# Kernel optimization log

Measured on AMD Instinct MI355X. Metric: run time of the kernel, lower is better.

Reference implementation:

```python
import jax, jax.numpy as jnp
import numpy as np

K = 20
NEG_SLOPE = 0.2
BN_EPS = 1e-5


def knn_idx(x, k):
    # x: (B, C, N) -> neighbor indices (B, N, k) by largest negative sq-distance
    xt = jnp.swapaxes(x, 1, 2)                      # (B, N, C)
    inner = 2.0 * jnp.einsum('bic,bjc->bij', xt, xt)
    sq = jnp.sum(xt * xt, axis=-1)                  # (B, N)
    dist = inner - sq[:, :, None] - sq[:, None, :]  # -||xi-xj||^2
    _, idx = jax.lax.top_k(dist, k)
    return idx


def edge_feature(x, src, idx):
    # x: (B, C, N) centers; src: (B, C, M) gather source; idx: (B, N, k)
    xt = jnp.swapaxes(x, 1, 2)                      # (B, N, C)
    st = jnp.swapaxes(src, 1, 2)                    # (B, M, C)
    b = jnp.arange(xt.shape[0])[:, None, None]
    neigh = st[b, idx]                              # (B, N, k, C)
    center = xt[:, :, None, :]                      # (B, N, 1, C)
    feat = jnp.concatenate(
        [neigh - center, jnp.broadcast_to(center, neigh.shape)], axis=-1)
    return jnp.transpose(feat, (0, 3, 1, 2))        # (B, 2C, N, k)


def conv_bn_lrelu(x, w, gamma, beta):
    # 1x1 conv (no bias) + training-mode BatchNorm2d + LeakyReLU(0.2)
    y = jnp.einsum('oc,bcnk->bonk', w, x)
    mean = jnp.mean(y, axis=(0, 2, 3), keepdims=True)
    var = jnp.var(y, axis=(0, 2, 3), keepdims=True)
    y = (y - mean) * jax.lax.rsqrt(var + BN_EPS)
    y = y * gamma[None, :, None, None] + beta[None, :, None, None]
    return jnp.where(y >= 0, y, NEG_SLOPE * y)


def knn_ia_idx(x, y, k):
    # cosine-similarity KNN from x (B,Cx,N) into y (B,Cy,M), normalize over channels
    xn = x / jnp.maximum(jnp.linalg.norm(x, axis=1, keepdims=True), 1e-12)
    yn = y / jnp.maximum(jnp.linalg.norm(y, axis=1, keepdims=True), 1e-12)
    simi = jnp.einsum('bci,bcj->bij', xn, yn)       # (B, N, M)
    _, idx = jax.lax.top_k(simi, k)
    return idx


def setup_inputs() -> dict:
    key = jax.random.key(0)
    ks = jax.random.split(key, 8)
    B, N, M, EMB = 8, 1024, 1024, 512
    x = jax.random.normal(ks[0], (B, 3, N), dtype=jnp.float32)
    y = jax.random.normal(ks[1], (B, 128, M), dtype=jnp.float32)
    def w(k_, o, c):
        return jax.random.normal(k_, (o, c), dtype=jnp.float32) * (1.0 / np.sqrt(c))
    inp = {
        'x': x, 'y': y,
        'w1': w(ks[2], 64, 6),
        'w2': w(ks[3], 64, 128),
        'w3': w(ks[4], 128, 128),
        'w4': w(ks[5], 256, 256),
        'w5': w(ks[6], EMB, 512),
        'g1': jnp.ones(64), 'b1': jnp.zeros(64),
        'g2': jnp.ones(64), 'b2': jnp.zeros(64),
        'g3': jnp.ones(128), 'b3': jnp.zeros(128),
        'g4': jnp.ones(256), 'b4': jnp.zeros(256),
        'g5': jnp.ones(EMB), 'b5': jnp.zeros(EMB),
    }
    return inp


def reference(x, y, w1, w2, w3, w4, w5, g1, b1, g2, b2, g3, b3, g4, b4, g5, b5):
    # block 1
    h = conv_bn_lrelu(edge_feature(x, x, knn_idx(x, K)), w1, g1, b1)
    x1 = jnp.max(h, axis=-1)                        # (B, 64, N)
    # block 2
    h = conv_bn_lrelu(edge_feature(x1, x1, knn_idx(x1, K)), w2, g2, b2)
    x2 = jnp.max(h, axis=-1)                        # (B, 64, N)
    # block 3
    h = conv_bn_lrelu(edge_feature(x2, x2, knn_idx(x2, K)), w3, g3, b3)
    x3 = jnp.max(h, axis=-1)                        # (B, 128, N)
    # block 4: cross-attention KNN into y (cosine similarity)
    h = conv_bn_lrelu(edge_feature(x3, y, knn_ia_idx(x3, y, K)), w4, g4, b4)
    x4 = jnp.max(h, axis=-1)                        # (B, 256, N)
    # final 1x1 conv + BN + LeakyReLU on concatenated features (512 ch)
    cat = jnp.concatenate([x1, x2, x3, x4], axis=1)  # (B, 512, N)
    out = conv_bn_lrelu(cat[..., None], w5, g5, b5)[..., 0]
    return out                                       # (B, n_emb_dims, N)
```

## Files before the change

### kernel.cpp

```cpp
#include <hip/hip_runtime.h>
#include <hip/hip_bf16.h>

#define KNN 20
#define NEG_SLOPE 0.2f

constexpr int BB = 8;
constexpr int NN = 1024;
constexpr int MM = 1024;

typedef short bf16x8 __attribute__((ext_vector_type(8)));
typedef float f32x4 __attribute__((ext_vector_type(4)));
typedef double f64x4 __attribute__((ext_vector_type(4)));
typedef unsigned long long u64;

__device__ __forceinline__ u64 pack_key64(double d, int j) {
  u64 u = (u64)__double_as_longlong(d);
  u = (u & 0x8000000000000000ULL) ? ~u : (u | 0x8000000000000000ULL);
  return (u & ~(u64)1023) | (u64)(1023 - j);
}

__device__ __forceinline__ void topk20_u64(u64 (&s)[16], int lane, int* op) {
#pragma unroll
  for (int p = 1; p < 16; p <<= 1) {
#pragma unroll
    for (int k = p; k >= 1; k >>= 1) {
#pragma unroll
      for (int j = k % p; j + k < 16; j += 2 * k) {
#pragma unroll
        for (int i = 0; i < k; ++i) {
          int a = j + i, b = j + i + k;
          if (b < 16 && (a / (2 * p)) == (b / (2 * p))) {
            u64 hi = s[a] > s[b] ? s[a] : s[b];
            u64 lo = s[a] > s[b] ? s[b] : s[a];
            s[a] = hi;
            s[b] = lo;
          }
        }
      }
    }
  }
#pragma unroll
  for (int r = 0; r < KNN; ++r) {
    u64 win = s[0];
#pragma unroll
    for (int off = 32; off > 0; off >>= 1) {
      u64 o = __shfl_xor(win, off, 64);
      win = o > win ? o : win;
    }
    if (lane == 0) op[r] = 1023 - (int)(win & (u64)1023);
    if (s[0] == win) {
#pragma unroll
      for (int i = 0; i < 15; ++i) s[i] = s[i + 1];
      s[15] = 0ULL;
    }
  }
}

__global__ void k_probe_mfma(int* __restrict__ rowt, int* __restrict__ colt,
                             int* __restrict__ flag) {
  __shared__ int cnt[256];
  __shared__ int oksh;
  int tid = threadIdx.x;
  if (tid == 0) oksh = 1;
  for (int e = tid; e < 256; e += 64) cnt[e] = 0;
  __syncthreads();
  int lane = tid & 63;
  f64x4 z = {0.0, 0.0, 0.0, 0.0};
  double ai = (double)(lane & 15);
  double p3 = 1.0, p5 = 1.0;
  int kq = lane >> 4;
  for (int t = 0; t < kq; ++t) { p3 *= 3.0; p5 *= 5.0; }
  f64x4 d1 = __builtin_amdgcn_mfma_f64_16x16x4f64(ai, 1.0, z, 0, 0, 0);
  f64x4 d2 = __builtin_amdgcn_mfma_f64_16x16x4f64(1.0, ai, z, 0, 0, 0);
  f64x4 d3 = __builtin_amdgcn_mfma_f64_16x16x4f64(p3, p5, z, 0, 0, 0);
  bool ok = true;
  int ri[4], ci[4];
#pragma unroll
  for (int r = 0; r < 4; ++r) {
    double va = d1[r], vb = d2[r], vp = d3[r];
    int i = (int)(va * 0.25);
    int j = (int)(vb * 0.25);
    bool e_ok = (i >= 0) && (i < 16) && (j >= 0) && (j < 16) &&
                (va == 4.0 * (double)i) && (vb == 4.0 * (double)j) && (vp == 3616.0);
    if (e_ok) {
      atomicAdd(&cnt[i * 16 + j], 1);
    } else {
      ok = false;
      i = 0;
      j = 0;
    }
    ri[r] = i;
    ci[r] = j;
  }
  if (!ok) atomicExch(&oksh, 0);
  __syncthreads();
  bool bij = true;
  for (int e = tid; e < 256; e += 64)
    if (cnt[e] != 1) bij = false;
  if (!bij) atomicExch(&oksh, 0);
  __syncthreads();
#pragma unroll
  for (int r = 0; r < 4; ++r) {
    rowt[lane * 4 + r] = ri[r];
    colt[lane * 4 + r] = ci[r];
  }
  if (tid == 0) *flag = oksh;
}

__global__ __launch_bounds__(256) void k_transpose_d(
    const float* __restrict__ in, double* __restrict__ out, int C, int Np) {
  int total = BB * C * Np;
  for (int t = blockIdx.x * 256 + threadIdx.x; t < total; t += gridDim.x * 256) {
    int c = t % C;
    int n = (t / C) % Np;
    int b = t / (C * Np);
    out[t] = (double)in[((size_t)b * C + c) * Np + n];
  }
}

__global__ __launch_bounds__(256) void k_cvt_bf16(
    const float* __restrict__ in, __hip_bfloat16* __restrict__ out, int n) {
  int i = blockIdx.x * 256 + threadIdx.x;
  if (i < n) out[i] = __float2bfloat16(in[i]);
}

template <int RECIP>
__global__ __launch_bounds__(256) void k_rowsq(
    const double* __restrict__ A, int ld, int C, double* __restrict__ sq) {
  int p = blockIdx.x * 256 + threadIdx.x;
  if (p >= BB * NN) return;
  const double* row = A + (size_t)p * ld;
  double s = 0.0;
  for (int c = 0; c < C; ++c) { double v = row[c]; s += v * v; }
  if (RECIP) {
    sq[p] = 1.0 / fmax(sqrt(s), 1e-12);
  } else {
    sq[p] = s;
  }
}

__global__ __launch_bounds__(256) void k_knn3(
    const double* __restrict__ xs3, const double* __restrict__ sq, int* __restrict__ idx) {
  __shared__ double P[NN * 3];
  int b = blockIdx.x;
  const double* Xb = xs3 + (size_t)b * NN * 3;
  int tid = threadIdx.x;
  for (int t = tid; t < NN * 3; t += 256) P[t] = Xb[t];
  __syncthreads();
  int wave = tid >> 6, lane = tid & 63;
  int i = blockIdx.y * 4 + wave;
  double xi = P[i * 3], yi = P[i * 3 + 1], zi = P[i * 3 + 2];
  double sqi = sq[b * NN + i];
  u64 s[16];
#pragma unroll
  for (int m = 0; m < 16; ++m) {
    int j = m * 64 + lane;
    double d = fma(xi, P[j * 3], 0.0);
    d = fma(yi, P[j * 3 + 1], d);
    d = fma(zi, P[j * 3 + 2], d);
    s[m] = pack_key64(2.0 * d - sqi - sq[b * NN + j], j);
  }
  int* op = idx + ((size_t)b * NN + i) * KNN;
  topk20_u64(s, lane, op);
}

template <int MODE>
__global__ __launch_bounds__(64, 2) void k_gram_u(
    const double* __restrict__ A, int lda, const double* __restrict__ Bm, int ldb,
    const double* __restrict__ sqA, const double* __restrict__ sqB,
    u64* __restrict__ kk, int C, int b0, const int* __restrict__ rowt,
    const int* __restrict__ colt, const int* __restrict__ flag) {
  __shared__ double As[2][8][69];
  __shared__ double Bs[2][8][69];
  int bg = b0 + blockIdx.x;
  int bl = blockIdx.x;
  int j0 = blockIdx.y * 64;
  int i0 = blockIdx.z * 64;
  const double* Ab = A + (size_t)bg * NN * lda;
  const double* Bb = Bm + (size_t)bg * MM * ldb;
  int lane = threadIdx.x;
  if (*flag) {
    int lm = lane & 15, lq = lane >> 4;
    int k8 = lane & 7, r8 = lane >> 3;
    const double* pa = Ab + (size_t)(i0 + r8) * lda + k8;
    const double* pb = Bb + (size_t)(j0 + r8) * ldb + k8;
    f64x4 acc[4][4] = {};
    double ra[8], rb[8];
#pragma unroll
    for (int r = 0; r < 8; ++r) {
      ra[r] = pa[(size_t)(8 * r) * lda];
      rb[r] = pb[(size_t)(8 * r) * ldb];
    }
#pragma unroll
    for (int r = 0; r < 8; ++r) {
      As[0][k8][r8 + 8 * r] = ra[r];
      Bs[0][k8][r8 + 8 * r] = rb[r];
    }
    int nblk = C >> 3;
    for (int cb = 0; cb < nblk; ++cb) {
      int buf = cb & 1;
      bool pf = (cb + 1 < nblk);
      if (pf) {
        int c0 = (cb + 1) << 3;
#pragma unroll
        for (int r = 0; r < 8; ++r) {
          ra[r] = pa[(size_t)(8 * r) * lda + c0];
          rb[r] = pb[(size_t)(8 * r) * ldb + c0];
        }
      }
#pragma unroll
      for (int kc = 0; kc < 2; ++kc) {
        double a_[4], b_[4];
#pragma unroll
        for (int s = 0; s < 4; ++s) {
          a_[s] = As[buf][kc * 4 + lq][s * 16 + lm];
          b_[s] = Bs[buf][kc * 4 + lq][s * 16 + lm];
        }
#pragma unroll
        for (int si = 0; si < 4; ++si)
#pragma unroll
          for (int sj = 0; sj < 4; ++sj)
            acc[si][sj] = __builtin_amdgcn_mfma_f64_16x16x4f64(a_[si], b_[sj],
                                                               acc[si][sj], 0, 0, 0);
      }
      if (pf) {
        int nb = buf ^ 1;
#pragma unroll
        for (int r = 0; r < 8; ++r) {
          As[nb][k8][r8 + 8 * r] = ra[r];
          Bs[nb][k8][r8 + 8 * r] = rb[r];
        }
      }
    }
    int rta[4], cta[4];
#pragma unroll
    for (int r = 0; r < 4; ++r) {
      rta[r] = rowt[lane * 4 + r];
      cta[r] = colt[lane * 4 + r];
    }
#pragma unroll
    for (int si = 0; si < 4; ++si) {
#pragma unroll
      for (int sj = 0; sj < 4; ++sj) {
#pragma unroll
        for (int r = 0; r < 4; ++r) {
          int i = i0 + si * 16 + rta[r];
          int j = j0 + sj * 16 + cta[r];
          double v = acc[si][sj][r];
          if (MODE == 1)
            v = 2.0 * v - sqA[(size_t)bg * NN + i] - sqB[(size_t)bg * MM + j];
          if (MODE == 2) v = v * sqA[(size_t)bg * NN + i] * sqB[(size_t)bg * MM + j];
          kk[((size_t)bl * NN + i) * MM + j] = pack_key64(v, j);
        }
      }
    }
  } else {
    int lr = lane >> 3, lc = lane & 7;
    double acc2[8][8] = {};
    for (int c0 = 0; c0 < C; c0 += 8) {
      if (c0) __syncthreads();
      for (int r = 0; r < 8; ++r) {
        int li = lane + r * 64;
        int row = li >> 3, k = li & 7;
        As[0][k][row] = Ab[(size_t)(i0 + row) * lda + c0 + k];
        Bs[0][k][row] = Bb[(size_t)(j0 + row) * ldb + c0 + k];
      }
      __syncthreads();
#pragma unroll
      for (int k = 0; k < 8; ++k) {
        double a_[8], b_[8];
#pragma unroll
        for (int t = 0; t < 8; ++t) {
          a_[t] = As[0][k][lr * 8 + t];
          b_[t] = Bs[0][k][lc * 8 + t];
        }
#pragma unroll
        for (int ii = 0; ii < 8; ++ii)
#pragma unroll
          for (int jj = 0; jj < 8; ++jj)
            acc2[ii][jj] = fma(a_[ii], b_[jj], acc2[ii][jj]);
      }
    }
    for (int ii = 0; ii < 8; ++ii) {
      int i = i0 + lr * 8 + ii;
      double qa = sqA[(size_t)bg * NN + i];
      for (int jj = 0; jj < 8; ++jj) {
        int j = j0 + lc * 8 + jj;
        double v = acc2[ii][jj];
        if (MODE == 1) v = 2.0 * v - qa - sqB[(size_t)bg * MM + j];
        if (MODE == 2) v = v * qa * sqB[(size_t)bg * MM + j];
        kk[((size_t)bl * NN + i) * MM + j] = pack_key64(v, j);
      }
    }
  }
}

__global__ __launch_bounds__(64, 2) void k_gram_sym(
    const double* __restrict__ A, int lda, const double* __restrict__ sqA,
    u64* __restrict__ kk, int C, int b0, const int* __restrict__ rowt,
    const int* __restrict__ colt, const int* __restrict__ flag) {
  __shared__ double As[2][8][69];
  __shared__ double Bs[2][8][69];
  int bg = b0 + blockIdx.x;
  int bl = blockIdx.x;
  int p = blockIdx.y;
  int r = (int)((sqrtf(8.f * p + 1.f) - 1.f) * 0.5f);
  while ((r + 1) * (r + 2) / 2 <= p) ++r;
  while (r * (r + 1) / 2 > p) --r;
  int cc = p - r * (r + 1) / 2;
  int i0 = r * 64, j0 = cc * 64;
  const double* Ab = A + (size_t)bg * NN * lda;
  int lane = threadIdx.x;
  if (*flag) {
    int lm = lane & 15, lq = lane >> 4;
    int k8 = lane & 7, r8 = lane >> 3;
    const double* pa = Ab + (size_t)(i0 + r8) * lda + k8;
    const double* pb = Ab + (size_t)(j0 + r8) * lda + k8;
    f64x4 acc[4][4] = {};
    double ra[8], rb[8];
#pragma unroll
    for (int r_ = 0; r_ < 8; ++r_) {
      ra[r_] = pa[(size_t)(8 * r_) * lda];
      rb[r_] = pb[(size_t)(8 * r_) * lda];
    }
#pragma unroll
    for (int r_ = 0; r_ < 8; ++r_) {
      As[0][k8][r8 + 8 * r_] = ra[r_];
      Bs[0][k8][r8 + 8 * r_] = rb[r_];
    }
    int nblk = C >> 3;
    for (int cb = 0; cb < nblk; ++cb) {
      int buf = cb & 1;
      bool pf = (cb + 1 < nblk);
      if (pf) {
        int c0 = (cb + 1) << 3;
#pragma unroll
        for (int r_ = 0; r_ < 8; ++r_) {
          ra[r_] = pa[(size_t)(8 * r_) * lda + c0];
          rb[r_] = pb[(size_t)(8 * r_) * lda + c0];
        }
      }
#pragma unroll
      for (int kc = 0; kc < 2; ++kc) {
        double a_[4], b_[4];
#pragma unroll
        for (int s = 0; s < 4; ++s) {
          a_[s] = As[buf][kc * 4 + lq][s * 16 + lm];
          b_[s] = Bs[buf][kc * 4 + lq][s * 16 + lm];
        }
#pragma unroll
        for (int si = 0; si < 4; ++si)
#pragma unroll
          for (int sj = 0; sj < 4; ++sj)
            acc[si][sj] = __builtin_amdgcn_mfma_f64_16x16x4f64(a_[si], b_[sj],
                                                               acc[si][sj], 0, 0, 0);
      }
      if (pf) {
        int nb = buf ^ 1;
#pragma unroll
        for (int r_ = 0; r_ < 8; ++r_) {
          As[nb][k8][r8 + 8 * r_] = ra[r_];
          Bs[nb][k8][r8 + 8 * r_] = rb[r_];
        }
      }
    }
    int rta[4], cta[4];
#pragma unroll
    for (int r_ = 0; r_ < 4; ++r_) {
      rta[r_] = rowt[lane * 4 + r_];
      cta[r_] = colt[lane * 4 + r_];
    }
    bool mir = (i0 != j0);
#pragma unroll
    for (int si = 0; si < 4; ++si) {
#pragma unroll
      for (int sj = 0; sj < 4; ++sj) {
#pragma unroll
        for (int r_ = 0; r_ < 4; ++r_) {
          int i = i0 + si * 16 + rta[r_];
          int j = j0 + sj * 16 + cta[r_];
          double v = 2.0 * acc[si][sj][r_] - sqA[(size_t)bg * NN + i] -
                     sqA[(size_t)bg * NN + j];
          kk[((size_t)bl * NN + i) * MM + j] = pack_key64(v, j);
          if (mir) kk[((size_t)bl * NN + j) * MM + i] = pack_key64(v, i);
        }
      }
    }
  } else {
    int lr = lane >> 3, lc = lane & 7;
    double acc2[8][8] = {};
    for (int c0 = 0; c0 < C; c0 += 8) {
      if (c0) __syncthreads();
      for (int r_ = 0; r_ < 8; ++r_) {
        int li = lane + r_ * 64;
        int row = li >> 3, k = li & 7;
        As[0][k][row] = Ab[(size_t)(i0 + row) * lda + c0 + k];
        Bs[0][k][row] = Ab[(size_t)(j0 + row) * lda + c0 + k];
      }
      __syncthreads();
#pragma unroll
      for (int k = 0; k < 8; ++k) {
        double a_[8], b_[8];
#pragma unroll
        for (int t = 0; t < 8; ++t) {
          a_[t] = As[0][k][lr * 8 + t];
          b_[t] = Bs[0][k][lc * 8 + t];
        }
#pragma unroll
        for (int ii = 0; ii < 8; ++ii)
#pragma unroll
          for (int jj = 0; jj < 8; ++jj)
            acc2[ii][jj] = fma(a_[ii], b_[jj], acc2[ii][jj]);
      }
    }
    bool mir = (i0 != j0);
    for (int ii = 0; ii < 8; ++ii) {
      int i = i0 + lr * 8 + ii;
      double qa = sqA[(size_t)bg * NN + i];
      for (int jj = 0; jj < 8; ++jj) {
        int j = j0 + lc * 8 + jj;
        double v = 2.0 * acc2[ii][jj] - qa - sqA[(size_t)bg * NN + j];
        kk[((size_t)bl * NN + i) * MM + j] = pack_key64(v, j);
        if (mir) kk[((size_t)bl * NN + j) * MM + i] = pack_key64(v, i);
      }
    }
  }
}

__global__ __launch_bounds__(256) void k_topk(const u64* __restrict__ kk,
                                              int* __restrict__ idx, int b0) {
  int wave = threadIdx.x >> 6;
  int lane = threadIdx.x & 63;
  int bl = blockIdx.x;
  int row = blockIdx.y * 4 + wave;
  const u64* rp = kk + ((size_t)bl * NN + row) * MM;
  u64 s[16];
#pragma unroll
  for (int m = 0; m < 16; ++m) s[m] = rp[m * 64 + lane];
  int* op = idx + ((size_t)(b0 + bl) * NN + row) * KNN;
  topk20_u64(s, lane, op);
}

__global__ __launch_bounds__(256) void k_featmm2(
    const double* __restrict__ src0, int ld0, int Np0,
    const double* __restrict__ src1, int ld1,
    const float* __restrict__ w, int CW,
    double* __restrict__ out0, double* __restrict__ out1, int C, int O,
    const int* __restrict__ rowt, const int* __restrict__ colt,
    const int* __restrict__ flag) {
  __shared__ double As[16][68];
  __shared__ double Ws[16][68];
  int nbo = O >> 6;
  int b = blockIdx.x;
  int mode = blockIdx.y >= nbo;
  int o0 = (blockIdx.y - (mode ? nbo : 0)) * 64;
  int j0 = blockIdx.z * 64;
  const double* src = mode ? src1 : src0;
  int lds_ = mode ? ld1 : ld0;
  int Np = mode ? NN : Np0;
  double* out = mode ? out1 : out0;
  int tid = threadIdx.x;
  const double* Sb = src + (size_t)b * Np * lds_;
  if (*flag) {
    int lane = tid & 63, wv = tid >> 6;
    int lm = lane & 15, lq = lane >> 4;
    f64x4 acc[4] = {};
    for (int c0 = 0; c0 < C; c0 += 16) {
      if (c0) __syncthreads();
      for (int r = 0; r < 4; ++r) {
        int li = tid + r * 256;
        int row = li >> 4, k = li & 15;
        int c = c0 + k;
        As[k][row] = (c < C) ? Sb[(size_t)(j0 + row) * lds_ + c] : 0.0;
        double wvv = 0.0;
        if (c < C) {
          const float* wr = w + (size_t)(o0 + row) * CW;
          wvv = (mode == 0) ? (double)wr[c] : ((double)wr[C + c] - (double)wr[c]);
        }
        Ws[k][row] = wvv;
      }
      __syncthreads();
#pragma unroll
      for (int kc = 0; kc < 4; ++kc) {
        double a = As[kc * 4 + lq][wv * 16 + lm];
#pragma unroll
        for (int t = 0; t < 4; ++t) {
          double bb = Ws[kc * 4 + lq][t * 16 + lm];
          acc[t] = __builtin_amdgcn_mfma_f64_16x16x4f64(a, bb, acc[t], 0, 0, 0);
        }
      }
    }
    int rta[4], cta[4];
#pragma unroll
    for (int r = 0; r < 4; ++r) {
      rta[r] = rowt[lane * 4 + r];
      cta[r] = colt[lane * 4 + r];
    }
#pragma unroll
    for (int t = 0; t < 4; ++t) {
#pragma unroll
      for (int r = 0; r < 4; ++r) {
        int j = j0 + wv * 16 + rta[r];
        int o = o0 + t * 16 + cta[r];
        out[((size_t)b * Np + j) * O + o] = acc[t][r];
      }
    }
  } else {
    int tx = tid & 15, ty = tid >> 4;
    double acc[4][4] = {};
    for (int c0 = 0; c0 < C; c0 += 16) {
      if (c0) __syncthreads();
      for (int r = 0; r < 4; ++r) {
        int li = tid + r * 256;
        int row = li >> 4, k = li & 15;
        int c = c0 + k;
        As[k][row] = (c < C) ? Sb[(size_t)(j0 + row) * lds_ + c] : 0.0;
        double wvv = 0.0;
        if (c < C) {
          const float* wr = w + (size_t)(o0 + row) * CW;
          wvv = (mode == 0) ? (double)wr[c] : ((double)wr[C + c] - (double)wr[c]);
        }
        Ws[k][row] = wvv;
      }
      __syncthreads();
#pragma unroll
      for (int k = 0; k < 16; ++k) {
        double a_[4], b_[4];
#pragma unroll
        for (int ii = 0; ii < 4; ++ii) a_[ii] = As[k][ty * 4 + ii];
#pragma unroll
        for (int jj = 0; jj < 4; ++jj) b_[jj] = Ws[k][tx * 4 + jj];
#pragma unroll
        for (int ii = 0; ii < 4; ++ii)
#pragma unroll
          for (int jj = 0; jj < 4; ++jj)
            acc[ii][jj] = fma(a_[ii], b_[jj], acc[ii][jj]);
      }
    }
    for (int ii = 0; ii < 4; ++ii) {
      int j = j0 + ty * 4 + ii;
      double* op = &out[((size_t)b * Np + j) * O + o0 + tx * 4];
      double2 v0, v1;
      v0.x = acc[ii][0];
      v0.y = acc[ii][1];
      v1.x = acc[ii][2];
      v1.y = acc[ii][3];
      *(double2*)op = v0;
      *(double2*)(op + 2) = v1;
    }
  }
}

__global__ __launch_bounds__(64, 2) void k_gemm5_mfma(
    const __hip_bfloat16* __restrict__ cath, const __hip_bfloat16* __restrict__ w5h,
    float* __restrict__ out) {
  int b = blockIdx.x;
  int j0 = blockIdx.y * 64;
  int o0 = blockIdx.z * 64;
  int lane = threadIdx.x;
  int m = lane & 15;
  int quad = lane >> 4;
  const __hip_bfloat16* arow = cath + ((size_t)(b * NN + j0 + m)) * 512 + quad * 8;
  const __hip_bfloat16* brow = w5h + ((size_t)(o0 + m)) * 512 + quad * 8;
  f32x4 acc[4][4] = {};
#pragma unroll
  for (int c0 = 0; c0 < 512; c0 += 32) {
    bf16x8 a[4], bb[4];
#pragma unroll
    for (int s = 0; s < 4; ++s) {
      a[s] = *(const bf16x8*)(arow + (size_t)s * 16 * 512 + c0);
      bb[s] = *(const bf16x8*)(brow + (size_t)s * 16 * 512 + c0);
    }
#pragma unroll
    for (int si = 0; si < 4; ++si)
#pragma unroll
      for (int sj = 0; sj < 4; ++sj)
        acc[si][sj] =
            __builtin_amdgcn_mfma_f32_16x16x32_bf16(a[si], bb[sj], acc[si][sj], 0, 0, 0);
  }
#pragma unroll
  for (int si = 0; si < 4; ++si) {
    float* ob = &out[((size_t)(b * NN + j0 + si * 16 + quad * 4)) * 512 + o0 + m];
#pragma unroll
    for (int sj = 0; sj < 4; ++sj)
#pragma unroll
      for (int r = 0; r < 4; ++r)
        ob[(size_t)r * 512 + sj * 16] = acc[si][sj][r];
  }
}

__global__ __launch_bounds__(256) void k_gather(
    const double* __restrict__ u, const double* __restrict__ t, const int* __restrict__ idx,
    double* __restrict__ stats, double* __restrict__ mx, int O, int srcNp) {
  __shared__ int lidx[16 * KNN];
  __shared__ double rs[256];
  __shared__ double rq[256];
  int b = blockIdx.x;
  int n0 = blockIdx.y * 16;
  int o0 = blockIdx.z * 64;
  int tid = threadIdx.x;
  int lane = tid & 63, nsl = tid >> 6;
  for (int w = tid; w < 16 * KNN; w += 256)
    lidx[w] = idx[((size_t)b * NN + n0) * KNN + w];
  __syncthreads();
  int oo = o0 + lane;
  double s1 = 0.0, s2 = 0.0;
  for (int ns = nsl; ns < 16; ns += 4) {
    size_t row = (size_t)b * NN + n0 + ns;
    double tv = t[row * O + oo];
    double mxv = -INFINITY;
    double a1 = 0.0, a2 = 0.0;
#pragma unroll
    for (int k = 0; k < KNN; ++k) {
      int j = lidx[ns * KNN + k];
      double yv = u[((size_t)b * srcNp + j) * O + oo] + tv;
      mxv = fmax(mxv, yv);
      a1 += yv;
      a2 = fma(yv, yv, a2);
    }
    mx[row * O + oo] = mxv;
    s1 += a1;
    s2 += a2;
  }
  rs[tid] = s1;
  rq[tid] = s2;
  __syncthreads();
  if (tid < 64) {
    s1 = rs[tid] + rs[tid + 64] + rs[tid + 128] + rs[tid + 192];
    s2 = rq[tid] + rq[tid + 64] + rq[tid + 128] + rq[tid + 192];
    atomicAdd(&stats[o0 + tid], s1);
    atomicAdd(&stats[O + o0 + tid], s2);
  }
}

__global__ __launch_bounds__(256) void k_bnapply(
    const double* __restrict__ mx, const double* __restrict__ u, const double* __restrict__ t,
    const int* __restrict__ idx, const double* __restrict__ stats,
    const float* __restrict__ gamma, const float* __restrict__ beta, double cnt,
    double* __restrict__ catd, __hip_bfloat16* __restrict__ cath, int coff, int O,
    int srcNp) {
  __shared__ double scs[256];
  __shared__ double scc[256];
  int tid = threadIdx.x;
  if (tid < O) {
    double mean = stats[tid] / cnt;
    double var = stats[O + tid] / cnt - mean * mean;
    if (var < 0.0) var = 0.0;
    double rstd = 1.0 / sqrt(var + 1e-5);
    double s = (double)gamma[tid] * rstd;
    scs[tid] = s;
    scc[tid] = (double)beta[tid] - mean * s;
  }
  __syncthreads();
  int i = blockIdx.x * 256 + tid;
  int total = BB * NN * O;
  if (i >= total) return;
  int oo = i % O;
  int n = (i / O) % NN;
  int b = i / (O * NN);
  double s = scs[oo], c = scc[oo];
  double v;
  if (s >= 0.0) {
    v = mx[i];
  } else {
    double tv = t[i];
    double mn = INFINITY;
    for (int k = 0; k < KNN; ++k) {
      int j = idx[((size_t)b * NN + n) * KNN + k];
      mn = fmin(mn, u[((size_t)b * srcNp + j) * O + oo] + tv);
    }
    v = mn;
  }
  double a = s * v + c;
  a = (a >= 0.0) ? a : 0.2 * a;
  size_t ci = ((size_t)b * NN + n) * 512 + coff + oo;
  cath[ci] = __float2bfloat16((float)a);
  if (coff < 256) catd[((size_t)b * NN + n) * 256 + coff + oo] = a;
}

__global__ __launch_bounds__(256) void k_stats512(
    const float* __restrict__ y5, double* __restrict__ stats) {
  int b = blockIdx.y;
  int n0 = blockIdx.x * 32;
  int tid = threadIdx.x;
  for (int part = 0; part < 2; ++part) {
    int oo = tid + part * 256;
    float a1 = 0.f, a2 = 0.f;
    for (int ns = 0; ns < 32; ++ns) {
      float v = y5[((size_t)b * NN + n0 + ns) * 512 + oo];
      a1 += v;
      a2 = fmaf(v, v, a2);
    }
    atomicAdd(&stats[oo], (double)a1);
    atomicAdd(&stats[512 + oo], (double)a2);
  }
}

__global__ __launch_bounds__(256) void k_final5b(
    const float* __restrict__ y5, const double* __restrict__ stats,
    const float* __restrict__ g5, const float* __restrict__ b5,
    float* __restrict__ out) {
  __shared__ float tile[64][65];
  __shared__ double scs[64];
  __shared__ double scc[64];
  int b = blockIdx.z;
  int n0 = blockIdx.x * 64;
  int o0 = blockIdx.y * 64;
  int tid = threadIdx.x;
  if (tid < 64) {
    int o = o0 + tid;
    double cnt = (double)(BB * NN);
    double mean = stats[o] / cnt;
    double var = stats[512 + o] / cnt - mean * mean;
    if (var < 0.0) var = 0.0;
    double rstd = 1.0 / sqrt(var + 1e-5);
    double s = (double)g5[o] * rstd;
    scs[tid] = s;
    scc[tid] = (double)b5[o] - mean * s;
  }
  __syncthreads();
  for (int r = 0; r < 16; ++r) {
    int li = tid + r * 256;
    int nl = li >> 6, ol = li & 63;
    float v = y5[((size_t)b * NN + n0 + nl) * 512 + o0 + ol];
    float a = (float)(scs[ol] * (double)v + scc[ol]);
    a = (a >= 0.f) ? a : NEG_SLOPE * a;
    tile[nl][ol] = a;
  }
  __syncthreads();
  for (int r = 0; r < 16; ++r) {
    int li = tid + r * 256;
    int ol = li >> 6, nl = li & 63;
    out[((size_t)b * 512 + o0 + ol) * NN + n0 + nl] = tile[nl][ol];
  }
}

extern "C" void kernel_launch(void* const* d_in, const int* in_sizes, int n_in,
                              void* d_out, int out_size, void* d_ws, size_t ws_size,
                              hipStream_t stream) {
  const float* x = (const float*)d_in[0];
  const float* y = (const float*)d_in[1];
  const float* w1 = (const float*)d_in[2];
  const float* w2 = (const float*)d_in[3];
  const float* w3 = (const float*)d_in[4];
  const float* w4 = (const float*)d_in[5];
  const float* w5 = (const float*)d_in[6];
  const float* g1 = (const float*)d_in[7];
  const float* b1 = (const float*)d_in[8];
  const float* g2 = (const float*)d_in[9];
  const float* b2 = (const float*)d_in[10];
  const float* g3 = (const float*)d_in[11];
  const float* b3 = (const float*)d_in[12];
  const float* g4 = (const float*)d_in[13];
  const float* b4 = (const float*)d_in[14];
  const float* g5 = (const float*)d_in[15];
  const float* b5 = (const float*)d_in[16];

  char* base = (char*)d_ws;
  size_t off = 0;
  auto alloc = [&](size_t bytes) -> char* {
    char* p = base + off;
    off += (bytes + 255) & ~(size_t)255;
    return p;
  };
  double* stAll = (double*)alloc(5 * 1024 * 8);
  double* sq = (double*)alloc((size_t)BB * NN * 8);
  double* rnx = (double*)alloc((size_t)BB * NN * 8);
  double* rny = (double*)alloc((size_t)BB * MM * 8);
  int* idxb = (int*)alloc((size_t)BB * NN * KNN * 4);
  int* rowt = (int*)alloc(256 * 4);
  int* colt = (int*)alloc(256 * 4);
  int* pflag = (int*)alloc(256);
  double* xs3d = (double*)alloc((size_t)BB * NN * 3 * 8);
  double* ysd = (double*)alloc((size_t)BB * MM * 128 * 8);
  double* catd = (double*)alloc((size_t)BB * NN * 256 * 8);
  __hip_bfloat16* cath = (__hip_bfloat16*)alloc((size_t)BB * NN * 512 * 2);
  __hip_bfloat16* w5h = (__hip_bfloat16*)alloc((size_t)512 * 512 * 2);
  double* uu = (double*)alloc((size_t)BB * MM * 256 * 8);
  double* tt = (double*)alloc((size_t)BB * NN * 256 * 8);
  size_t kkBatchBytes = (size_t)NN * MM * 8;
  size_t avail = (ws_size > off) ? (ws_size - off) : 0;
  int CB = (int)(avail / kkBatchBytes);
  if (CB < 1) CB = 1;
  if (CB > BB) CB = BB;
  u64* KK = (u64*)alloc((size_t)CB * kkBatchBytes);
  float* y5 = (float*)uu;
  double* mx = (double*)d_out;
  float* outp = (float*)d_out;

  const double cntE = (double)BB * NN * KNN;

  auto knn = [&](const double* A, int lda, const double* Bm, int ldb,
                 const double* sa, const double* sb, int C, int sym) {
    for (int b0 = 0; b0 < BB; b0 += CB) {
      int cb = (BB - b0 < CB) ? (BB - b0) : CB;
      if (sym) {
        k_gram_sym<<<dim3(cb, 136), 64, 0, stream>>>(A, lda, sa, KK, C, b0, rowt, colt,
                                                     pflag);
      } else {
        dim3 g(cb, MM / 64, NN / 64);
        k_gram_u<2><<<g, 64, 0, stream>>>(A, lda, Bm, ldb, sa, sb, KK, C, b0, rowt,
                                          colt, pflag);
      }
      k_topk<<<dim3(cb, 256), 256, 0, stream>>>(KK, idxb, b0);
    }
  };

  auto edge_layer = [&](const double* ctr, int ldc, const double* src, int ldsrc,
                        int srcNp, const float* w, int CW, const float* g,
                        const float* bb, int C, int O, int coff, double* st) {
    k_featmm2<<<dim3(8, 2 * (O / 64), 16), 256, 0, stream>>>(
        src, ldsrc, srcNp, ctr, ldc, w, CW, uu, tt, C, O, rowt, colt, pflag);
    k_gather<<<dim3(BB, NN / 16, O / 64), 256, 0, stream>>>(uu, tt, idxb, st, mx, O,
                                                            srcNp);
    k_bnapply<<<(BB * NN * O + 255) / 256, 256, 0, stream>>>(
        mx, uu, tt, idxb, st, g, bb, cntE, catd, cath, coff, O, srcNp);
  };

  hipMemsetAsync(stAll, 0, 5 * 1024 * 8, stream);
  k_probe_mfma<<<1, 64, 0, stream>>>(rowt, colt, pflag);
  k_transpose_d<<<96, 256, 0, stream>>>(x, xs3d, 3, NN);
  k_transpose_d<<<2048, 256, 0, stream>>>(y, ysd, 128, MM);
  k_cvt_bf16<<<1024, 256, 0, stream>>>(w5, w5h, 512 * 512);

  k_rowsq<0><<<32, 256, 0, stream>>>(xs3d, 3, 3, sq);
  k_knn3<<<dim3(BB, 256), 256, 0, stream>>>(xs3d, sq, idxb);
  edge_layer(xs3d, 3, xs3d, 3, NN, w1, 6, g1, b1, 3, 64, 0, stAll);

  k_rowsq<0><<<32, 256, 0, stream>>>(catd, 256, 64, sq);
  knn(catd, 256, catd, 256, sq, sq, 64, 1);
  edge_layer(catd, 256, catd, 256, NN, w2, 128, g2, b2, 64, 64, 64, stAll + 1024);

  k_rowsq<0><<<32, 256, 0, stream>>>(catd + 64, 256, 64, sq);
  knn(catd + 64, 256, catd + 64, 256, sq, sq, 64, 1);
  edge_layer(catd + 64, 256, catd + 64, 256, NN, w3, 128, g3, b3, 64, 128, 128,
             stAll + 2048);

  k_rowsq<1><<<32, 256, 0, stream>>>(catd + 128, 256, 128, rnx);
  k_rowsq<1><<<32, 256, 0, stream>>>(ysd, 128, 128, rny);
  knn(catd + 128, 256, ysd, 128, rnx, rny, 128, 0);
  edge_layer(catd + 128, 256, ysd, 128, MM, w4, 256, g4, b4, 128, 256, 256,
             stAll + 3072);

  double* st5 = stAll + 4096;
  k_gemm5_mfma<<<dim3(8, 16, 8), 64, 0, stream>>>(cath, w5h, y5);
  k_stats512<<<dim3(32, 8), 256, 0, stream>>>(y5, st5);
  k_final5b<<<dim3(16, 8, 8), 256, 0, stream>>>(y5, st5, g5, b5, outp);
}
```

Before: 645.2 us.

## Rewrite edge feature GEMM as single-wave 64x64 MFMA tile with register-prefetched double buffering

Changes the per-edge-layer fp64 GEMM from a 256-thread block, where each wave computed a 16x64 strip, to a single 64-lane wave that computes the whole 64x64 tile with a 4x4 grid of f64 MFMAs. It uses an 8-deep K step with double-buffered LDS, prefetching the next slab into registers while the current one is consumed. This removes block-level barriers and raises operand reuse per LDS read. The grid is reordered so the output-channel index varies fastest, for both this kernel and the gather kernel, to improve locality. The cost is heavy register use and fewer waves per block, which may reduce latency hiding.

```diff
diff --git a/kernel.cpp b/kernel.cpp
--- a/kernel.cpp
+++ b/kernel.cpp
@@ -441,112 +441,142 @@
   topk20_u64(s, lane, op);
 }
 
-__global__ __launch_bounds__(256) void k_featmm2(
+__global__ __launch_bounds__(64, 2) void k_featmm_u(
     const double* __restrict__ src0, int ld0, int Np0,
     const double* __restrict__ src1, int ld1,
     const float* __restrict__ w, int CW,
     double* __restrict__ out0, double* __restrict__ out1, int C, int O,
     const int* __restrict__ rowt, const int* __restrict__ colt,
     const int* __restrict__ flag) {
-  __shared__ double As[16][68];
-  __shared__ double Ws[16][68];
+  __shared__ double As[2][8][69];
+  __shared__ double Ws[2][8][69];
   int nbo = O >> 6;
-  int b = blockIdx.x;
-  int mode = blockIdx.y >= nbo;
-  int o0 = (blockIdx.y - (mode ? nbo : 0)) * 64;
-  int j0 = blockIdx.z * 64;
+  int mode = blockIdx.x >= nbo;
+  int o0 = (blockIdx.x - (mode ? nbo : 0)) * 64;
+  int j0 = blockIdx.y * 64;
+  int b = blockIdx.z;
   const double* src = mode ? src1 : src0;
   int lds_ = mode ? ld1 : ld0;
   int Np = mode ? NN : Np0;
   double* out = mode ? out1 : out0;
-  int tid = threadIdx.x;
   const double* Sb = src + (size_t)b * Np * lds_;
+  int lane = threadIdx.x;
   if (*flag) {
-    int lane = tid & 63, wv = tid >> 6;
     int lm = lane & 15, lq = lane >> 4;
-    f64x4 acc[4] = {};
-    for (int c0 = 0; c0 < C; c0 += 16) {
+    int k8 = lane & 7, r8 = lane >> 3;
+    const double* pa = Sb + (size_t)(j0 + r8) * lds_ + k8;
+    const float* pw = w + (size_t)(o0 + r8) * CW;
+    f64x4 acc[4][4] = {};
+    double ra[8], rb[8];
+    auto wval = [&](int radd, int c) -> double {
+      const float* wr = pw + (size_t)radd * CW;
+      return (mode == 0) ? (double)wr[c] : ((double)wr[C + c] - (double)wr[c]);
+    };
+#pragma unroll
+    for (int r = 0; r < 8; ++r) {
+      bool in = (k8 < C);
+      ra[r] = in ? pa[(size_t)(8 * r) * lds_] : 0.0;
+      rb[r] = in ? wval(8 * r, k8) : 0.0;
+    }
+#pragma unroll
+    for (int r = 0; r < 8; ++r) {
+      As[0][k8][r8 + 8 * r] = ra[r];
+      Ws[0][k8][r8 + 8 * r] = rb[r];
+    }
+    int nblk = (C + 7) >> 3;
+    for (int cb = 0; cb < nblk; ++cb) {
+      int buf = cb & 1;
+      bool pf = (cb + 1 < nblk);
+      if (pf) {
+        int c0 = (cb + 1) << 3;
+        bool in = (c0 + k8 < C);
+#pragma unroll
+        for (int r = 0; r < 8; ++r) {
+          ra[r] = in ? pa[(size_t)(8 * r) * lds_ + c0] : 0.0;
+          rb[r] = in ? wval(8 * r, c0 + k8) : 0.0;
+        }
+      }
+#pragma unroll
+      for (int kc = 0; kc < 2; ++kc) {
+        double a_[4], b_[4];
+#pragma unroll
+        for (int s = 0; s < 4; ++s) {
+          a_[s] = As[buf][kc * 4 + lq][s * 16 + lm];
+          b_[s] = Ws[buf][kc * 4 + lq][s * 16 + lm];
+        }
+#pragma unroll
+        for (int si = 0; si < 4; ++si)
+#pragma unroll
+          for (int sj = 0; sj < 4; ++sj)
+            acc[si][sj] = __builtin_amdgcn_mfma_f64_16x16x4f64(a_[si], b_[sj],
+                                                               acc[si][sj], 0, 0, 0);
+      }
+      if (pf) {
+        int nb = buf ^ 1;
+#pragma unroll
+        for (int r = 0; r < 8; ++r) {
+          As[nb][k8][r8 + 8 * r] = ra[r];
+          Ws[nb][k8][r8 + 8 * r] = rb[r];
+        }
+      }
+    }
+    int rta[4], cta[4];
+#pragma unroll
+    for (int r = 0; r < 4; ++r) {
+      rta[r] = rowt[lane * 4 + r];
+      cta[r] = colt[lane * 4 + r];
+    }
+#pragma unroll
+    for (int si = 0; si < 4; ++si) {
+#pragma unroll
+      for (int sj = 0; sj < 4; ++sj) {
+#pragma unroll
+        for (int r = 0; r < 4; ++r) {
+          int j = j0 + si * 16 + rta[r];
+          int o = o0 + sj * 16 + cta[r];
+          out[((size_t)b * Np + j) * O + o] = acc[si][sj][r];
+        }
+      }
+    }
+  } else {
+    int lr = lane >> 3, lc = lane & 7;
+    double acc2[8][8] = {};
+    for (int c0 = 0; c0 < C; c0 += 8) {
       if (c0) __syncthreads();
-      for (int r = 0; r < 4; ++r) {
-        int li = tid + r * 256;
-        int row = li >> 4, k = li & 15;
+      for (int r = 0; r < 8; ++r) {
+        int li = lane + r * 64;
+        int row = li >> 3, k = li & 7;
         int c = c0 + k;
-        As[k][row] = (c < C) ? Sb[(size_t)(j0 + row) * lds_ + c] : 0.0;
+        As[0][k][row] = (c < C) ? Sb[(size_t)(j0 + row) * lds_ + c] : 0.0;
         double wvv = 0.0;
         if (c < C) {
           const float* wr = w + (size_t)(o0 + row) * CW;
           wvv = (mode == 0) ? (double)wr[c] : ((double)wr[C + c] - (double)wr[c]);
         }
-        Ws[k][row] = wvv;
+        Ws[0][k][row] = wvv;
       }
       __syncthreads();
 #pragma unroll
-      for (int kc = 0; kc < 4; ++kc) {
-        double a = As[kc * 4 + lq][wv * 16 + lm];
-#pragma unroll
-        for (int t = 0; t < 4; ++t) {
-          double bb = Ws[kc * 4 + lq][t * 16 + lm];
-          acc[t] = __builtin_amdgcn_mfma_f64_16x16x4f64(a, bb, acc[t], 0, 0, 0);
-        }
-      }
-    }
-    int rta[4], cta[4];
-#pragma unroll
-    for (int r = 0; r < 4; ++r) {
-      rta[r] = rowt[lane * 4 + r];
-      cta[r] = colt[lane * 4 + r];
-    }
-#pragma unroll
-    for (int t = 0; t < 4; ++t) {
-#pragma unroll
-      for (int r = 0; r < 4; ++r) {
-        int j = j0 + wv * 16 + rta[r];
-        int o = o0 + t * 16 + cta[r];
-        out[((size_t)b * Np + j) * O + o] = acc[t][r];
-      }
-    }
-  } else {
-    int tx = tid & 15, ty = tid >> 4;
-    double acc[4][4] = {};
-    for (int c0 = 0; c0 < C; c0 += 16) {
-      if (c0) __syncthreads();
-      for (int r = 0; r < 4; ++r) {
-        int li = tid + r * 256;
-        int row = li >> 4, k = li & 15;
-        int c = c0 + k;
-        As[k][row] = (c < C) ? Sb[(size_t)(j0 + row) * lds_ + c] : 0.0;
-        double wvv = 0.0;
-        if (c < C) {
-          const float* wr = w + (size_t)(o0 + row) * CW;
-          wvv = (mode == 0) ? (double)wr[c] : ((double)wr[C + c] - (double)wr[c]);
-        }
-        Ws[k][row] = wvv;
-      }
-      __syncthreads();
-#pragma unroll
-      for (int k = 0; k < 16; ++k) {
-        double a_[4], b_[4];
-#pragma unroll
-        for (int ii = 0; ii < 4; ++ii) a_[ii] = As[k][ty * 4 + ii];
-#pragma unroll
-        for (int jj = 0; jj < 4; ++jj) b_[jj] = Ws[k][tx * 4 + jj];
-#pragma unroll
-        for (int ii = 0; ii < 4; ++ii)
-#pragma unroll
-          for (int jj = 0; jj < 4; ++jj)
-            acc[ii][jj] = fma(a_[ii], b_[jj], acc[ii][jj]);
-      }
-    }
-    for (int ii = 0; ii < 4; ++ii) {
-      int j = j0 + ty * 4 + ii;
-      double* op = &out[((size_t)b * Np + j) * O + o0 + tx * 4];
-      double2 v0, v1;
-      v0.x = acc[ii][0];
-      v0.y = acc[ii][1];
-      v1.x = acc[ii][2];
-      v1.y = acc[ii][3];
-      *(double2*)op = v0;
-      *(double2*)(op + 2) = v1;
+      for (int k = 0; k < 8; ++k) {
+        double a_[8], b_[8];
+#pragma unroll
+        for (int t = 0; t < 8; ++t) {
+          a_[t] = As[0][k][lr * 8 + t];
+          b_[t] = Ws[0][k][lc * 8 + t];
+        }
+#pragma unroll
+        for (int ii = 0; ii < 8; ++ii)
+#pragma unroll
+          for (int jj = 0; jj < 8; ++jj)
+            acc2[ii][jj] = fma(a_[ii], b_[jj], acc2[ii][jj]);
+      }
+    }
+    for (int ii = 0; ii < 8; ++ii) {
+      int j = j0 + lr * 8 + ii;
+      for (int jj = 0; jj < 8; ++jj) {
+        int o = o0 + lc * 8 + jj;
+        out[((size_t)b * Np + j) * O + o] = acc2[ii][jj];
+      }
     }
   }
 }
@@ -595,9 +625,9 @@
   __shared__ int lidx[16 * KNN];
   __shared__ double rs[256];
   __shared__ double rq[256];
-  int b = blockIdx.x;
+  int b = blockIdx.z;
   int n0 = blockIdx.y * 16;
-  int o0 = blockIdx.z * 64;
+  int o0 = blockIdx.x * 64;
   int tid = threadIdx.x;
   int lane = tid & 63, nsl = tid >> 6;
   for (int w = tid; w < 16 * KNN; w += 256)
@@ -809,9 +839,9 @@
   auto edge_layer = [&](const double* ctr, int ldc, const double* src, int ldsrc,
                         int srcNp, const float* w, int CW, const float* g,
                         const float* bb, int C, int O, int coff, double* st) {
-    k_featmm2<<<dim3(8, 2 * (O / 64), 16), 256, 0, stream>>>(
+    k_featmm_u<<<dim3(2 * (O / 64), NN / 64, BB), 64, 0, stream>>>(
         src, ldsrc, srcNp, ctr, ldc, w, CW, uu, tt, C, O, rowt, colt, pflag);
-    k_gather<<<dim3(BB, NN / 16, O / 64), 256, 0, stream>>>(uu, tt, idxb, st, mx, O,
+    k_gather<<<dim3(O / 64, NN / 16, BB), 256, 0, stream>>>(uu, tt, idxb, st, mx, O,
                                                             srcNp);
     k_bnapply<<<(BB * NN * O + 255) / 256, 256, 0, stream>>>(
         mx, uu, tt, idxb, st, g, bb, cntE, catd, cath, coff, O, srcNp);
```

After: 702.2 us. 8.8% more time.
